# Kernel optimization log

Measured on AMD Instinct MI355X. Metric: run time of the kernel, lower is better.

## Reference

```python
import jax, jax.numpy as jnp
import numpy as np

N_NODES = 100_000
N_EDGES = 3_200_000
IN_FEAT = 512
HIDDEN = 16
N_CLASSES = 7


def setup_inputs() -> dict:
    key = jax.random.key(0)
    kx, ke, kw1, kw2 = jax.random.split(key, 4)
    x = jax.random.normal(kx, (N_NODES, IN_FEAT), dtype=jnp.float32)
    edge_index = jax.random.randint(ke, (2, N_EDGES), 0, N_NODES, dtype=jnp.int64)
    W1 = jax.random.normal(kw1, (IN_FEAT, HIDDEN), dtype=jnp.float32) * (1.0 / np.sqrt(IN_FEAT))
    b1 = jnp.zeros((HIDDEN,), dtype=jnp.float32)
    W2 = jax.random.normal(kw2, (HIDDEN, N_CLASSES), dtype=jnp.float32) * (1.0 / np.sqrt(HIDDEN))
    b2 = jnp.zeros((N_CLASSES,), dtype=jnp.float32)
    return {"x": x, "edge_index": edge_index, "W1": W1, "b1": b1, "W2": W2, "b2": b2}


def _gcn_conv(x, edge_index, W, b):
    """GCNConv: h = D^{-1/2} (A + I) D^{-1/2} (x W) + b  (symmetric normalization, self-loops)."""
    n = x.shape[0]
    h = x @ W  # transform first (small out dim), then aggregate
    loop = jnp.arange(n, dtype=edge_index.dtype)
    src = jnp.concatenate([edge_index[0], loop])  # message sources (incl. self-loops)
    dst = jnp.concatenate([edge_index[1], loop])  # message destinations
    deg = jax.ops.segment_sum(jnp.ones_like(dst, dtype=h.dtype), dst, num_segments=n)
    dinv = jnp.where(deg > 0, jax.lax.rsqrt(deg), 0.0).astype(h.dtype)
    norm = dinv[src] * dinv[dst]                 # [E+N]
    msg = h[src] * norm[:, None]                 # gather + scale
    out = jax.ops.segment_sum(msg, dst, num_segments=n)  # scatter-add
    return out + b


def reference(x, edge_index, W1, b1, W2, b2):
    h = jax.nn.relu(_gcn_conv(x, edge_index, W1, b1))
    # dropout is identity in eval mode
    logits = _gcn_conv(h, edge_index, W2, b2)
    return jax.nn.log_softmax(logits, axis=1)
```

## Files before the change

### kernel.cpp

```cpp
#include <hip/hip_runtime.h>
#include <math.h>

#define TPB 256
#define SCANT 1024

namespace {

constexpr int IN_FEAT = 512;
constexpr int HID = 16;

__device__ inline float4 shfl_xor4(float4 v, int m) {
  v.x = __shfl_xor(v.x, m);
  v.y = __shfl_xor(v.y, m);
  v.z = __shfl_xor(v.z, m);
  v.w = __shfl_xor(v.w, m);
  return v;
}

__global__ void k_detect(const int* __restrict__ ei32, int* __restrict__ flag) {
  __shared__ int red[TPB];
  int t = threadIdx.x;
  int v = 0;
  for (int i = t; i < 2048; i += TPB) v |= ei32[2 * i + 1];
  red[t] = v;
  __syncthreads();
  for (int s = TPB / 2; s > 0; s >>= 1) {
    if (t < s) red[t] |= red[t + s];
    __syncthreads();
  }
  if (t == 0) *flag = (red[0] == 0) ? 1 : 0;
}

__global__ void k_zero_i(int* __restrict__ p, int n) {
  int i = blockIdx.x * TPB + threadIdx.x;
  if (i < n) p[i] = 0;
}

__global__ __launch_bounds__(TPB) void k_binA(const int* __restrict__ ei32,
                                              const long long* __restrict__ ei64,
                                              const int* __restrict__ flag,
                                              int* __restrict__ bucketCnt, int E, int NB) {
  __shared__ int hist[1024];
  int t = threadIdx.x;
  for (int i = t; i < 1024; i += TPB) hist[i] = 0;
  __syncthreads();
  long long e0 = (long long)blockIdx.x * 8192;
  int use64 = *flag;
  for (int j = 0; j < 32; j++) {
    long long e = e0 + j * TPB + t;
    if (e < E) {
      int d = use64 ? (int)ei64[E + e] : ei32[E + e];
      atomicAdd(&hist[d >> 8], 1);
    }
  }
  __syncthreads();
  for (int b = t; b < NB; b += TPB) {
    int c = hist[b];
    if (c) atomicAdd(&bucketCnt[b], c);
  }
}

__global__ __launch_bounds__(SCANT) void k_binB(const int* __restrict__ bucketCnt,
                                                int* __restrict__ bucketBase,
                                                int* __restrict__ cursor,
                                                int* __restrict__ offsets, int n, int NB) {
  __shared__ int sb[SCANT];
  int t = threadIdx.x;
  int v = (t < NB) ? bucketCnt[t] : 0;
  sb[t] = v;
  __syncthreads();
  for (int off = 1; off < SCANT; off <<= 1) {
    int u = (t >= off) ? sb[t - off] : 0;
    __syncthreads();
    sb[t] += u;
    __syncthreads();
  }
  if (t < NB) {
    int base = sb[t] - v;
    bucketBase[t] = base;
    cursor[t] = base;
  }
  if (t == NB - 1) {
    bucketBase[NB] = sb[t];
    offsets[n] = sb[t];
  }
}

__global__ __launch_bounds__(TPB) void k_binC(const int* __restrict__ ei32,
                                              const long long* __restrict__ ei64,
                                              const int* __restrict__ flag,
                                              int* __restrict__ cursor,
                                              unsigned int* __restrict__ binned, int E, int NB) {
  __shared__ int cnt[1024];
  __shared__ int gbase[1024];
  int t = threadIdx.x;
  for (int i = t; i < 1024; i += TPB) cnt[i] = 0;
  __syncthreads();
  long long e0 = (long long)blockIdx.x * 8192;
  int use64 = *flag;
  for (int j = 0; j < 32; j++) {
    long long e = e0 + j * TPB + t;
    if (e < E) {
      int d = use64 ? (int)ei64[E + e] : ei32[E + e];
      atomicAdd(&cnt[d >> 8], 1);
    }
  }
  __syncthreads();
  for (int b = t; b < NB; b += TPB) {
    int c = cnt[b];
    gbase[b] = c ? atomicAdd(&cursor[b], c) : 0;
  }
  __syncthreads();
  for (int i = t; i < 1024; i += TPB) cnt[i] = 0;
  __syncthreads();
  for (int j = 0; j < 32; j++) {
    long long e = e0 + j * TPB + t;
    if (e < E) {
      int s, d;
      if (use64) {
        s = (int)ei64[e];
        d = (int)ei64[E + e];
      } else {
        s = ei32[e];
        d = ei32[(long long)E + e];
      }
      int b = d >> 8;
      int r = atomicAdd(&cnt[b], 1);
      binned[gbase[b] + r] = ((unsigned)(d & 255) << 24) | (unsigned)s;
    }
  }
}

__global__ __launch_bounds__(TPB) void k_binD(const int* __restrict__ bucketBase,
                                              const unsigned int* __restrict__ binned,
                                              int* __restrict__ offsets, float* __restrict__ dinv,
                                              int* __restrict__ csr, int n) {
  __shared__ int ncnt[256];
  __shared__ int nsc[256];
  __shared__ int ncur[256];
  int t = threadIdx.x;
  int b = blockIdx.x;
  int base = bucketBase[b];
  int cnt = bucketBase[b + 1] - base;
  ncnt[t] = 0;
  __syncthreads();
  for (int i = t; i < cnt; i += TPB) {
    unsigned p = binned[base + i];
    atomicAdd(&ncnt[p >> 24], 1);
  }
  __syncthreads();
  int c = ncnt[t];
  nsc[t] = c;
  __syncthreads();
  for (int off = 1; off < 256; off <<= 1) {
    int u = (t >= off) ? nsc[t - off] : 0;
    __syncthreads();
    nsc[t] += u;
    __syncthreads();
  }
  int excl = nsc[t] - c;
  int node = (b << 8) + t;
  if (node < n) {
    offsets[node] = base + excl;
    dinv[node] = rsqrtf((float)(c + 1));
  }
  ncur[t] = base + excl;
  __syncthreads();
  for (int i = t; i < cnt; i += TPB) {
    unsigned p = binned[base + i];
    int loc = (int)(p >> 24);
    int pos = atomicAdd(&ncur[loc], 1);
    csr[pos] = (int)(p & 0xFFFFFF);
  }
}

__global__ __launch_bounds__(TPB) void k_gemm1b(const float* __restrict__ x,
                                                const float* __restrict__ W1,
                                                const float* __restrict__ dinv,
                                                float* __restrict__ hs1, int n) {
  __shared__ float xs[192 * 64];
  __shared__ float wt[16 * 68];
  int t = threadIdx.x;
  int rq = t >> 2;
  int cq = t & 3;
  int R0 = blockIdx.x * 192;
  float acc[3][4];
#pragma unroll
  for (int i = 0; i < 3; i++)
#pragma unroll
    for (int c = 0; c < 4; c++) acc[i][c] = 0.f;

  const float4* x4 = (const float4*)x;
  for (int tile = 0; tile < 8; tile++) {
    int k04 = tile << 4;
#pragma unroll
    for (int p = 0; p < 12; p++) {
      int i = p * TPB + t;
      int rr = i >> 4, kk = i & 15;
      int row = R0 + rr;
      if (row > n - 1) row = n - 1;
      float4 v = x4[(long long)row * 128 + k04 + kk];
      *(float4*)&xs[((rr << 4) + (kk ^ (rr & 15))) << 2] = v;
    }
#pragma unroll
    for (int p = 0; p < 4; p++) {
      int i = p * TPB + t;
      int c = i & 15, kf = i >> 4;
      wt[c * 68 + kf] = W1[(((tile << 6) + kf) << 4) + c];
    }
    __syncthreads();
#pragma unroll 4
    for (int kk = 0; kk < 16; kk++) {
      float4 wv[4];
#pragma unroll
      for (int c = 0; c < 4; c++)
        wv[c] = *(const float4*)&wt[(cq * 4 + c) * 68 + (kk << 2)];
#pragma unroll
      for (int i = 0; i < 3; i++) {
        int rr = rq + (i << 6);
        float4 xv = *(const float4*)&xs[((rr << 4) + (kk ^ (rr & 15))) << 2];
#pragma unroll
        for (int c = 0; c < 4; c++) {
          acc[i][c] = fmaf(xv.x, wv[c].x, acc[i][c]);
          acc[i][c] = fmaf(xv.y, wv[c].y, acc[i][c]);
          acc[i][c] = fmaf(xv.z, wv[c].z, acc[i][c]);
          acc[i][c] = fmaf(xv.w, wv[c].w, acc[i][c]);
        }
      }
    }
    __syncthreads();
  }
#pragma unroll
  for (int i = 0; i < 3; i++) {
    int row = R0 + rq + (i << 6);
    if (row < n) {
      float di = dinv[row];
      float4 o = make_float4(acc[i][0] * di, acc[i][1] * di, acc[i][2] * di,
                             acc[i][3] * di);
      *(float4*)&hs1[(long long)row * HID + (cq << 2)] = o;
    }
  }
}

__global__ void k_agg1(const int* __restrict__ offsets, const int* __restrict__ csr,
                       const float* __restrict__ hs1, float* __restrict__ t1, int n) {
  int wid = (int)(((unsigned)blockIdx.x * TPB + threadIdx.x) >> 6);
  if (wid >= n) return;
  int lane = threadIdx.x & 63;
  int q = lane & 3;
  int eg = lane >> 2;
  int s0 = offsets[wid], s1 = offsets[wid + 1];
  float4 acc = make_float4(0.f, 0.f, 0.f, 0.f);
  for (int e = s0 + eg; e < s1; e += 16) {
    int s = csr[e];
    float4 v = *(const float4*)(hs1 + (long long)s * HID + (q << 2));
    acc.x += v.x; acc.y += v.y; acc.z += v.z; acc.w += v.w;
  }
  for (int m = 4; m < 64; m <<= 1) {
    float4 o = shfl_xor4(acc, m);
    acc.x += o.x; acc.y += o.y; acc.z += o.z; acc.w += o.w;
  }
  if (lane < 4) {
    float4 sv = *(const float4*)(hs1 + (long long)wid * HID + (lane << 2));
    acc.x += sv.x; acc.y += sv.y; acc.z += sv.z; acc.w += sv.w;
    *(float4*)(t1 + (long long)wid * HID + (lane << 2)) = acc;
  }
}

__global__ void k_layer2(const float* __restrict__ t1, const float* __restrict__ dinv,
                         const float* __restrict__ b1, const float* __restrict__ W2,
                         float* __restrict__ hs2, float* __restrict__ t2, int n) {
  int i = blockIdx.x * TPB + threadIdx.x;
  if (i >= n) return;
  float di = dinv[i];
  float h[16];
  const float4* tp = (const float4*)(t1 + (long long)i * 16);
#pragma unroll
  for (int q = 0; q < 4; q++) {
    float4 v = tp[q];
    float4 b = ((const float4*)b1)[q];
    h[4 * q + 0] = fmaxf(fmaf(di, v.x, b.x), 0.f);
    h[4 * q + 1] = fmaxf(fmaf(di, v.y, b.y), 0.f);
    h[4 * q + 2] = fmaxf(fmaf(di, v.z, b.z), 0.f);
    h[4 * q + 3] = fmaxf(fmaf(di, v.w, b.w), 0.f);
  }
  float o[8];
#pragma unroll
  for (int j = 0; j < 7; j++) {
    float s = 0.f;
#pragma unroll
    for (int cc = 0; cc < 16; cc++) s = fmaf(h[cc], W2[cc * 7 + j], s);
    o[j] = s * di;
  }
  o[7] = 0.f;
  float4 lo = make_float4(o[0], o[1], o[2], o[3]);
  float4 hi = make_float4(o[4], o[5], o[6], o[7]);
  float4* hp = (float4*)(hs2 + (long long)i * 8);
  hp[0] = lo; hp[1] = hi;
  if (t2) {
    float4* qp = (float4*)(t2 + (long long)i * 8);
    qp[0] = lo; qp[1] = hi;
  }
}

__global__ void k_agg2(const int* __restrict__ offsets, const int* __restrict__ csr,
                       const float* __restrict__ hs2, const float* __restrict__ dinv,
                       const float* __restrict__ b2, float* __restrict__ out, int n) {
  int wid = (int)(((unsigned)blockIdx.x * TPB + threadIdx.x) >> 6);
  if (wid >= n) return;
  int lane = threadIdx.x & 63;
  int q = lane & 1;
  int eg = lane >> 1;
  int s0 = offsets[wid], s1 = offsets[wid + 1];
  float4 acc = make_float4(0.f, 0.f, 0.f, 0.f);
  for (int e = s0 + eg; e < s1; e += 32) {
    int s = csr[e];
    float4 v = *(const float4*)(hs2 + (long long)s * 8 + (q << 2));
    acc.x += v.x; acc.y += v.y; acc.z += v.z; acc.w += v.w;
  }
  for (int m = 2; m < 64; m <<= 1) {
    float4 o = shfl_xor4(acc, m);
    acc.x += o.x; acc.y += o.y; acc.z += o.z; acc.w += o.w;
  }
  float4 sv = *(const float4*)(hs2 + (long long)wid * 8 + (q << 2));
  acc.x += sv.x; acc.y += sv.y; acc.z += sv.z; acc.w += sv.w;
  float di = dinv[wid];
  int f0 = q << 2;
  float vx = fmaf(di, acc.x, b2[f0 + 0]);
  float vy = fmaf(di, acc.y, b2[f0 + 1]);
  float vz = fmaf(di, acc.z, b2[f0 + 2]);
  float vw = (q == 0) ? fmaf(di, acc.w, b2[3]) : 0.f;
  float vw_eff = (q == 0) ? vw : -1e30f;
  float mloc = fmaxf(fmaxf(vx, vy), fmaxf(vz, vw_eff));
  float mm = fmaxf(mloc, __shfl_xor(mloc, 1));
  float sl = expf(vx - mm) + expf(vy - mm) + expf(vz - mm) +
             ((q == 0) ? expf(vw - mm) : 0.f);
  float ss = sl + __shfl_xor(sl, 1);
  float lse = mm + logf(ss);
  if (lane < 2) {
    long long base = (long long)wid * 7 + (q << 2);
    out[base + 0] = vx - lse;
    out[base + 1] = vy - lse;
    out[base + 2] = vz - lse;
    if (q == 0) out[base + 3] = vw - lse;
  }
}

__global__ void k_hist(const int* __restrict__ ei32, const long long* __restrict__ ei64,
                       const int* __restrict__ flag, int* __restrict__ cnt, int E) {
  int e = blockIdx.x * TPB + threadIdx.x;
  if (e >= E) return;
  int d = (*flag) ? (int)ei64[(long long)E + e] : ei32[(long long)E + e];
  atomicAdd(&cnt[d], 1);
}

__global__ __launch_bounds__(SCANT) void k_scan(int* __restrict__ cnt_cursor,
                                                int* __restrict__ offsets,
                                                float* __restrict__ dinv, int n) {
  __shared__ int sb[SCANT];
  int t = threadIdx.x;
  int chunk = (n + SCANT - 1) / SCANT;
  int lo = t * chunk;
  int hi = lo + chunk;
  if (lo > n) lo = n;
  if (hi > n) hi = n;
  int s = 0;
  for (int i = lo; i < hi; i++) s += cnt_cursor[i];
  sb[t] = s;
  __syncthreads();
  for (int off = 1; off < SCANT; off <<= 1) {
    int v = (t >= off) ? sb[t - off] : 0;
    __syncthreads();
    sb[t] += v;
    __syncthreads();
  }
  int run = sb[t] - s;
  for (int i = lo; i < hi; i++) {
    int c = cnt_cursor[i];
    offsets[i] = run;
    cnt_cursor[i] = run;
    dinv[i] = rsqrtf((float)(c + 1));
    run += c;
  }
  if (hi == n && lo < n) offsets[n] = run;
}

__global__ void k_build(const int* __restrict__ ei32, const long long* __restrict__ ei64,
                        const int* __restrict__ flag, int* __restrict__ cursor,
                        int* __restrict__ csr, int E) {
  int e = blockIdx.x * TPB + threadIdx.x;
  if (e >= E) return;
  int s, d;
  if (*flag) {
    s = (int)ei64[e];
    d = (int)ei64[(long long)E + e];
  } else {
    s = ei32[e];
    d = ei32[(long long)E + e];
  }
  int pos = atomicAdd(&cursor[d], 1);
  csr[pos] = s;
}

__global__ __launch_bounds__(TPB) void k_gemm1(const float* __restrict__ x,
                                               const float* __restrict__ W1,
                                               const float* __restrict__ dinv,
                                               float* __restrict__ hs1,
                                               float* __restrict__ t1, int n) {
  __shared__ float Wt[HID * IN_FEAT];
  __shared__ float xsl[16 * IN_FEAT];
  int t = threadIdx.x;
  for (int i = t; i < IN_FEAT * HID; i += TPB) {
    int k = i >> 4, c = i & 15;
    int pk = (k >> 2) ^ (c & 7);
    Wt[c * IN_FEAT + (pk << 2) + (k & 3)] = W1[i];
  }
  int c = t >> 4, r = t & 15;
  int xsw = r & 7, wsw = c & 7;
  int ntiles = (n + 15) >> 4;
  for (int tile = blockIdx.x; tile < ntiles; tile += gridDim.x) {
    int r0 = tile << 4;
    for (int i = t; i < 16 * (IN_FEAT / 4); i += TPB) {
      int rr = i >> 7, kk = i & 127;
      int row = r0 + rr;
      if (row > n - 1) row = n - 1;
      float4 v = ((const float4*)x)[(long long)row * (IN_FEAT / 4) + kk];
      *(float4*)&xsl[rr * IN_FEAT + ((kk ^ (rr & 7)) << 2)] = v;
    }
    __syncthreads();
    float acc = 0.f;
#pragma unroll 8
    for (int kk = 0; kk < IN_FEAT / 4; kk++) {
      float4 xv = *(const float4*)&xsl[r * IN_FEAT + ((kk ^ xsw) << 2)];
      float4 wv = *(const float4*)&Wt[c * IN_FEAT + ((kk ^ wsw) << 2)];
      acc = fmaf(xv.x, wv.x, acc);
      acc = fmaf(xv.y, wv.y, acc);
      acc = fmaf(xv.z, wv.z, acc);
      acc = fmaf(xv.w, wv.w, acc);
    }
    int row = r0 + r;
    if (row < n) {
      float val = acc * dinv[row];
      hs1[(long long)row * HID + c] = val;
      if (t1) t1[(long long)row * HID + c] = val;
    }
    __syncthreads();
  }
}

__global__ void k_deg_init(float* __restrict__ deg, int n) {
  int i = blockIdx.x * TPB + threadIdx.x;
  if (i < n) deg[i] = 1.0f;
}

__global__ void k_deg_accum(const int* __restrict__ ei32, const long long* __restrict__ ei64,
                            const int* __restrict__ flag, float* __restrict__ deg, int E) {
  int e = blockIdx.x * TPB + threadIdx.x;
  if (e >= E) return;
  int d = (*flag) ? (int)ei64[(long long)E + e] : ei32[(long long)E + e];
  atomicAdd(&deg[d], 1.0f);
}

__global__ void k_rsqrt(float* __restrict__ deg, int n) {
  int i = blockIdx.x * TPB + threadIdx.x;
  if (i < n) deg[i] = rsqrtf(deg[i]);
}

__global__ void k_scatter1(const int* __restrict__ ei32, const long long* __restrict__ ei64,
                           const int* __restrict__ flag, const float* __restrict__ hs1,
                           float* __restrict__ t1, int E) {
  long long gid = (long long)blockIdx.x * TPB + threadIdx.x;
  long long e = gid >> 4;
  if (e >= E) return;
  int f = (int)(gid & 15);
  int s, d;
  if (*flag) {
    s = (int)ei64[e];
    d = (int)ei64[E + e];
  } else {
    s = ei32[e];
    d = ei32[(long long)E + e];
  }
  atomicAdd(&t1[(long long)d * HID + f], hs1[(long long)s * HID + f]);
}

__global__ void k_scatter2(const int* __restrict__ ei32, const long long* __restrict__ ei64,
                           const int* __restrict__ flag, const float* __restrict__ hs2,
                           float* __restrict__ t2, int E) {
  long long gid = (long long)blockIdx.x * TPB + threadIdx.x;
  long long e = gid >> 3;
  if (e >= E) return;
  int f = (int)(gid & 7);
  if (f == 7) return;
  int s, d;
  if (*flag) {
    s = (int)ei64[e];
    d = (int)ei64[E + e];
  } else {
    s = ei32[e];
    d = ei32[(long long)E + e];
  }
  atomicAdd(&t2[(long long)d * 8 + f], hs2[(long long)s * 8 + f]);
}

__global__ void k_final(const float* __restrict__ t2, const float* __restrict__ dinv,
                        const float* __restrict__ b2, float* __restrict__ out, int n) {
  int i = blockIdx.x * TPB + threadIdx.x;
  if (i >= n) return;
  float di = dinv[i];
  float v[7];
  float m = -1e30f;
#pragma unroll
  for (int j = 0; j < 7; j++) {
    v[j] = fmaf(di, t2[(long long)i * 8 + j], b2[j]);
    m = fmaxf(m, v[j]);
  }
  float s = 0.f;
#pragma unroll
  for (int j = 0; j < 7; j++) s += expf(v[j] - m);
  float lse = m + logf(s);
#pragma unroll
  for (int j = 0; j < 7; j++) out[(long long)i * 7 + j] = v[j] - lse;
}

}

extern "C" void kernel_launch(void* const* d_in, const int* in_sizes, int n_in,
                              void* d_out, int out_size, void* d_ws, size_t ws_size,
                              hipStream_t stream) {
  const float* x = (const float*)d_in[0];
  const int* ei32 = (const int*)d_in[1];
  const long long* ei64 = (const long long*)d_in[1];
  const float* W1 = (const float*)d_in[2];
  const float* b1 = (const float*)d_in[3];
  const float* W2 = (const float*)d_in[4];
  const float* b2 = (const float*)d_in[5];
  float* out = (float*)d_out;

  int n = in_sizes[0] / IN_FEAT;
  int E = in_sizes[1] / 2;

  int nb_n = (n + TPB - 1) / TPB;
  int nb_e = (E + TPB - 1) / TPB;
  int nb_w = (n + 3) / 4;
  int nb_g = (n + 191) / 192;
  int NB = (n + 255) >> 8;
  int NCH = (int)(((long long)E + 8191) / 8192);

  float* ws = (float*)d_ws;
  int* flag = (int*)d_ws;
  auto align16 = [](long long v) { return (v + 15) & ~15LL; };

  long long w = 64;
  float* dinv = ws + w; w = align16(w + n);
  int* offsets = (int*)(ws + w); w = align16(w + n + 1);
  int* bucketCnt = (int*)(ws + w); w = align16(w + NB);
  int* bucketBase = (int*)(ws + w); w = align16(w + NB + 1);
  int* cursor = (int*)(ws + w); w = align16(w + NB);
  unsigned int* binned = (unsigned int*)(ws + w); w = align16(w + E);
  int* csr = (int*)(ws + w); w = align16(w + E);
  float* hs1 = ws + w; w = align16(w + (long long)n * HID);
  float* t1 = ws + w; w = align16(w + (long long)n * HID);
  float* hs2 = ws + w; w = align16(w + (long long)n * 8);
  bool bin_ok = (NB >= 1) && (NB <= 1024) && (n <= (1 << 24)) &&
                (ws_size >= (size_t)w * 4);

  long long w2l = 64;
  float* dinv_c = ws + w2l; w2l = align16(w2l + n);
  int* offsets_c = (int*)(ws + w2l); w2l = align16(w2l + n + 1);
  int* cursor_c = (int*)(ws + w2l); w2l = align16(w2l + n);
  int* csr_c = (int*)(ws + w2l); w2l = align16(w2l + E);
  float* hs1_c = ws + w2l; w2l = align16(w2l + (long long)n * HID);
  float* t1_c = ws + w2l; w2l = align16(w2l + (long long)n * HID);
  float* hs2_c = ws + w2l; w2l = align16(w2l + (long long)n * 8);
  bool csr_ok = (ws_size >= (size_t)w2l * 4);

  if (bin_ok) {
    int nb_nb = (NB + TPB - 1) / TPB;
    hipLaunchKernelGGL(k_detect, dim3(1), dim3(TPB), 0, stream, ei32, flag);
    hipLaunchKernelGGL(k_zero_i, dim3(nb_nb), dim3(TPB), 0, stream, bucketCnt, NB);
    hipLaunchKernelGGL(k_binA, dim3(NCH), dim3(TPB), 0, stream, ei32, ei64, flag, bucketCnt, E, NB);
    hipLaunchKernelGGL(k_binB, dim3(1), dim3(SCANT), 0, stream, bucketCnt, bucketBase, cursor,
                       offsets, n, NB);
    hipLaunchKernelGGL(k_binC, dim3(NCH), dim3(TPB), 0, stream, ei32, ei64, flag, cursor, binned,
                       E, NB);
    hipLaunchKernelGGL(k_binD, dim3(NB), dim3(TPB), 0, stream, bucketBase, binned, offsets, dinv,
                       csr, n);
    hipLaunchKernelGGL(k_gemm1b, dim3(nb_g), dim3(TPB), 0, stream, x, W1, dinv, hs1, n);
    hipLaunchKernelGGL(k_agg1, dim3(nb_w), dim3(TPB), 0, stream, offsets, csr, hs1, t1, n);
    hipLaunchKernelGGL(k_layer2, dim3(nb_n), dim3(TPB), 0, stream, t1, dinv, b1, W2, hs2,
                       (float*)nullptr, n);
    hipLaunchKernelGGL(k_agg2, dim3(nb_w), dim3(TPB), 0, stream, offsets, csr, hs2, dinv, b2,
                       out, n);
  } else if (csr_ok) {
    hipLaunchKernelGGL(k_detect, dim3(1), dim3(TPB), 0, stream, ei32, flag);
    hipLaunchKernelGGL(k_zero_i, dim3(nb_n), dim3(TPB), 0, stream, cursor_c, n);
    hipLaunchKernelGGL(k_hist, dim3(nb_e), dim3(TPB), 0, stream, ei32, ei64, flag, cursor_c, E);
    hipLaunchKernelGGL(k_scan, dim3(1), dim3(SCANT), 0, stream, cursor_c, offsets_c, dinv_c, n);
    hipLaunchKernelGGL(k_build, dim3(nb_e), dim3(TPB), 0, stream, ei32, ei64, flag, cursor_c,
                       csr_c, E);
    hipLaunchKernelGGL(k_gemm1b, dim3(nb_g), dim3(TPB), 0, stream, x, W1, dinv_c, hs1_c, n);
    hipLaunchKernelGGL(k_agg1, dim3(nb_w), dim3(TPB), 0, stream, offsets_c, csr_c, hs1_c, t1_c, n);
    hipLaunchKernelGGL(k_layer2, dim3(nb_n), dim3(TPB), 0, stream, t1_c, dinv_c, b1, W2, hs2_c,
                       (float*)nullptr, n);
    hipLaunchKernelGGL(k_agg2, dim3(nb_w), dim3(TPB), 0, stream, offsets_c, csr_c, hs2_c, dinv_c,
                       b2, out, n);
  } else {
    float* dinv_f = ws + 64;
    float* hs1_f = dinv_f + n;
    float* t1_f = hs1_f + (long long)n * HID;
    float* hs2_f = t1_f + (long long)n * HID;
    float* t2_f = hs2_f + (long long)n * 8;
    long long w1s = (long long)E * 16, w2s = (long long)E * 8;
    int nb_s1 = (int)((w1s + TPB - 1) / TPB);
    int nb_s2 = (int)((w2s + TPB - 1) / TPB);
    hipLaunchKernelGGL(k_detect, dim3(1), dim3(TPB), 0, stream, ei32, flag);
    hipLaunchKernelGGL(k_deg_init, dim3(nb_n), dim3(TPB), 0, stream, dinv_f, n);
    hipLaunchKernelGGL(k_deg_accum, dim3(nb_e), dim3(TPB), 0, stream, ei32, ei64, flag, dinv_f, E);
    hipLaunchKernelGGL(k_rsqrt, dim3(nb_n), dim3(TPB), 0, stream, dinv_f, n);
    hipLaunchKernelGGL(k_gemm1, dim3(1024), dim3(TPB), 0, stream, x, W1, dinv_f, hs1_f, t1_f, n);
    hipLaunchKernelGGL(k_scatter1, dim3(nb_s1), dim3(TPB), 0, stream, ei32, ei64, flag, hs1_f,
                       t1_f, E);
    hipLaunchKernelGGL(k_layer2, dim3(nb_n), dim3(TPB), 0, stream, t1_f, dinv_f, b1, W2, hs2_f,
                       t2_f, n);
    hipLaunchKernelGGL(k_scatter2, dim3(nb_s2), dim3(TPB), 0, stream, ei32, ei64, flag, hs2_f,
                       t2_f, E);
    hipLaunchKernelGGL(k_final, dim3(nb_n), dim3(TPB), 0, stream, t2_f, dinv_f, b2, out, n);
  }
}
```

Measured before the change: 523.5 us.

## Aggregate directly from bucketed edges with LDS atomics, dropping CSR build

Replaces the per-node CSR construction (k_binD) with a lighter degree-only kernel and switches the bucket size from 256 to 128 nodes. Both aggregation passes now read the bucket-binned edge list directly and accumulate into shared-memory tiles with LDS float atomics. The layer-2 transform is fused into the first aggregation, and log-softmax into the second. This removes the CSR scatter pass, the t1 buffer and the separate layer2 launch, at the cost of shared-memory atomic contention and nondeterministic float summation order.

```diff
diff --git a/kernel.cpp b/kernel.cpp
--- a/kernel.cpp
+++ b/kernel.cpp
@@ -8,14 +8,8 @@
 
 constexpr int IN_FEAT = 512;
 constexpr int HID = 16;
-
-__device__ inline float4 shfl_xor4(float4 v, int m) {
-  v.x = __shfl_xor(v.x, m);
-  v.y = __shfl_xor(v.y, m);
-  v.z = __shfl_xor(v.z, m);
-  v.w = __shfl_xor(v.w, m);
-  return v;
-}
+constexpr int BSH = 7;
+constexpr int BSZ = 128;
 
 __global__ void k_detect(const int* __restrict__ ei32, int* __restrict__ flag) {
   __shared__ int red[TPB];
@@ -50,7 +44,7 @@
     long long e = e0 + j * TPB + t;
     if (e < E) {
       int d = use64 ? (int)ei64[E + e] : ei32[E + e];
-      atomicAdd(&hist[d >> 8], 1);
+      atomicAdd(&hist[d >> BSH], 1);
     }
   }
   __syncthreads();
@@ -62,8 +56,7 @@
 
 __global__ __launch_bounds__(SCANT) void k_binB(const int* __restrict__ bucketCnt,
                                                 int* __restrict__ bucketBase,
-                                                int* __restrict__ cursor,
-                                                int* __restrict__ offsets, int n, int NB) {
+                                                int* __restrict__ cursor, int NB) {
   __shared__ int sb[SCANT];
   int t = threadIdx.x;
   int v = (t < NB) ? bucketCnt[t] : 0;
@@ -80,10 +73,7 @@
     bucketBase[t] = base;
     cursor[t] = base;
   }
-  if (t == NB - 1) {
-    bucketBase[NB] = sb[t];
-    offsets[n] = sb[t];
-  }
+  if (t == NB - 1) bucketBase[NB] = sb[t];
 }
 
 __global__ __launch_bounds__(TPB) void k_binC(const int* __restrict__ ei32,
@@ -102,7 +92,7 @@
     long long e = e0 + j * TPB + t;
     if (e < E) {
       int d = use64 ? (int)ei64[E + e] : ei32[E + e];
-      atomicAdd(&cnt[d >> 8], 1);
+      atomicAdd(&cnt[d >> BSH], 1);
     }
   }
   __syncthreads();
@@ -124,54 +114,26 @@
         s = ei32[e];
         d = ei32[(long long)E + e];
       }
-      int b = d >> 8;
+      int b = d >> BSH;
       int r = atomicAdd(&cnt[b], 1);
-      binned[gbase[b] + r] = ((unsigned)(d & 255) << 24) | (unsigned)s;
-    }
-  }
-}
-
-__global__ __launch_bounds__(TPB) void k_binD(const int* __restrict__ bucketBase,
+      binned[gbase[b] + r] = ((unsigned)(d & (BSZ - 1)) << 25) | (unsigned)s;
+    }
+  }
+}
+
+__global__ __launch_bounds__(TPB) void k_dinv(const int* __restrict__ bucketBase,
                                               const unsigned int* __restrict__ binned,
-                                              int* __restrict__ offsets, float* __restrict__ dinv,
-                                              int* __restrict__ csr, int n) {
-  __shared__ int ncnt[256];
-  __shared__ int nsc[256];
-  __shared__ int ncur[256];
-  int t = threadIdx.x;
-  int b = blockIdx.x;
+                                              float* __restrict__ dinv, int n) {
+  __shared__ int ncnt[BSZ];
+  int t = threadIdx.x, b = blockIdx.x;
   int base = bucketBase[b];
   int cnt = bucketBase[b + 1] - base;
-  ncnt[t] = 0;
-  __syncthreads();
-  for (int i = t; i < cnt; i += TPB) {
-    unsigned p = binned[base + i];
-    atomicAdd(&ncnt[p >> 24], 1);
-  }
-  __syncthreads();
-  int c = ncnt[t];
-  nsc[t] = c;
-  __syncthreads();
-  for (int off = 1; off < 256; off <<= 1) {
-    int u = (t >= off) ? nsc[t - off] : 0;
-    __syncthreads();
-    nsc[t] += u;
-    __syncthreads();
-  }
-  int excl = nsc[t] - c;
-  int node = (b << 8) + t;
-  if (node < n) {
-    offsets[node] = base + excl;
-    dinv[node] = rsqrtf((float)(c + 1));
-  }
-  ncur[t] = base + excl;
-  __syncthreads();
-  for (int i = t; i < cnt; i += TPB) {
-    unsigned p = binned[base + i];
-    int loc = (int)(p >> 24);
-    int pos = atomicAdd(&ncur[loc], 1);
-    csr[pos] = (int)(p & 0xFFFFFF);
-  }
+  if (t < BSZ) ncnt[t] = 0;
+  __syncthreads();
+  for (int i = t; i < cnt; i += TPB) atomicAdd(&ncnt[binned[base + i] >> 25], 1);
+  __syncthreads();
+  int node = (b << BSH) + t;
+  if (t < BSZ && node < n) dinv[node] = rsqrtf((float)(ncnt[t] + 1));
 }
 
 __global__ __launch_bounds__(TPB) void k_gemm1b(const float* __restrict__ x,
@@ -242,164 +204,106 @@
   }
 }
 
-__global__ void k_agg1(const int* __restrict__ offsets, const int* __restrict__ csr,
-                       const float* __restrict__ hs1, float* __restrict__ t1, int n) {
-  int wid = (int)(((unsigned)blockIdx.x * TPB + threadIdx.x) >> 6);
-  if (wid >= n) return;
-  int lane = threadIdx.x & 63;
-  int q = lane & 3;
-  int eg = lane >> 2;
-  int s0 = offsets[wid], s1 = offsets[wid + 1];
-  float4 acc = make_float4(0.f, 0.f, 0.f, 0.f);
-  for (int e = s0 + eg; e < s1; e += 16) {
-    int s = csr[e];
-    float4 v = *(const float4*)(hs1 + (long long)s * HID + (q << 2));
-    acc.x += v.x; acc.y += v.y; acc.z += v.z; acc.w += v.w;
-  }
-  for (int m = 4; m < 64; m <<= 1) {
-    float4 o = shfl_xor4(acc, m);
-    acc.x += o.x; acc.y += o.y; acc.z += o.z; acc.w += o.w;
-  }
-  if (lane < 4) {
-    float4 sv = *(const float4*)(hs1 + (long long)wid * HID + (lane << 2));
-    acc.x += sv.x; acc.y += sv.y; acc.z += sv.z; acc.w += sv.w;
-    *(float4*)(t1 + (long long)wid * HID + (lane << 2)) = acc;
-  }
-}
-
-__global__ void k_layer2(const float* __restrict__ t1, const float* __restrict__ dinv,
-                         const float* __restrict__ b1, const float* __restrict__ W2,
-                         float* __restrict__ hs2, float* __restrict__ t2, int n) {
-  int i = blockIdx.x * TPB + threadIdx.x;
-  if (i >= n) return;
-  float di = dinv[i];
-  float h[16];
-  const float4* tp = (const float4*)(t1 + (long long)i * 16);
-#pragma unroll
-  for (int q = 0; q < 4; q++) {
-    float4 v = tp[q];
-    float4 b = ((const float4*)b1)[q];
-    h[4 * q + 0] = fmaxf(fmaf(di, v.x, b.x), 0.f);
-    h[4 * q + 1] = fmaxf(fmaf(di, v.y, b.y), 0.f);
-    h[4 * q + 2] = fmaxf(fmaf(di, v.z, b.z), 0.f);
-    h[4 * q + 3] = fmaxf(fmaf(di, v.w, b.w), 0.f);
-  }
-  float o[8];
-#pragma unroll
-  for (int j = 0; j < 7; j++) {
-    float s = 0.f;
-#pragma unroll
-    for (int cc = 0; cc < 16; cc++) s = fmaf(h[cc], W2[cc * 7 + j], s);
-    o[j] = s * di;
-  }
-  o[7] = 0.f;
-  float4 lo = make_float4(o[0], o[1], o[2], o[3]);
-  float4 hi = make_float4(o[4], o[5], o[6], o[7]);
-  float4* hp = (float4*)(hs2 + (long long)i * 8);
-  hp[0] = lo; hp[1] = hi;
-  if (t2) {
-    float4* qp = (float4*)(t2 + (long long)i * 8);
-    qp[0] = lo; qp[1] = hi;
-  }
-}
-
-__global__ void k_agg2(const int* __restrict__ offsets, const int* __restrict__ csr,
-                       const float* __restrict__ hs2, const float* __restrict__ dinv,
-                       const float* __restrict__ b2, float* __restrict__ out, int n) {
-  int wid = (int)(((unsigned)blockIdx.x * TPB + threadIdx.x) >> 6);
-  if (wid >= n) return;
-  int lane = threadIdx.x & 63;
-  int q = lane & 1;
-  int eg = lane >> 1;
-  int s0 = offsets[wid], s1 = offsets[wid + 1];
-  float4 acc = make_float4(0.f, 0.f, 0.f, 0.f);
-  for (int e = s0 + eg; e < s1; e += 32) {
-    int s = csr[e];
-    float4 v = *(const float4*)(hs2 + (long long)s * 8 + (q << 2));
-    acc.x += v.x; acc.y += v.y; acc.z += v.z; acc.w += v.w;
-  }
-  for (int m = 2; m < 64; m <<= 1) {
-    float4 o = shfl_xor4(acc, m);
-    acc.x += o.x; acc.y += o.y; acc.z += o.z; acc.w += o.w;
-  }
-  float4 sv = *(const float4*)(hs2 + (long long)wid * 8 + (q << 2));
-  acc.x += sv.x; acc.y += sv.y; acc.z += sv.z; acc.w += sv.w;
-  float di = dinv[wid];
-  int f0 = q << 2;
-  float vx = fmaf(di, acc.x, b2[f0 + 0]);
-  float vy = fmaf(di, acc.y, b2[f0 + 1]);
-  float vz = fmaf(di, acc.z, b2[f0 + 2]);
-  float vw = (q == 0) ? fmaf(di, acc.w, b2[3]) : 0.f;
-  float vw_eff = (q == 0) ? vw : -1e30f;
-  float mloc = fmaxf(fmaxf(vx, vy), fmaxf(vz, vw_eff));
-  float mm = fmaxf(mloc, __shfl_xor(mloc, 1));
-  float sl = expf(vx - mm) + expf(vy - mm) + expf(vz - mm) +
-             ((q == 0) ? expf(vw - mm) : 0.f);
-  float ss = sl + __shfl_xor(sl, 1);
-  float lse = mm + logf(ss);
-  if (lane < 2) {
-    long long base = (long long)wid * 7 + (q << 2);
-    out[base + 0] = vx - lse;
-    out[base + 1] = vy - lse;
-    out[base + 2] = vz - lse;
-    if (q == 0) out[base + 3] = vw - lse;
-  }
-}
-
-__global__ void k_hist(const int* __restrict__ ei32, const long long* __restrict__ ei64,
-                       const int* __restrict__ flag, int* __restrict__ cnt, int E) {
-  int e = blockIdx.x * TPB + threadIdx.x;
-  if (e >= E) return;
-  int d = (*flag) ? (int)ei64[(long long)E + e] : ei32[(long long)E + e];
-  atomicAdd(&cnt[d], 1);
-}
-
-__global__ __launch_bounds__(SCANT) void k_scan(int* __restrict__ cnt_cursor,
-                                                int* __restrict__ offsets,
-                                                float* __restrict__ dinv, int n) {
-  __shared__ int sb[SCANT];
-  int t = threadIdx.x;
-  int chunk = (n + SCANT - 1) / SCANT;
-  int lo = t * chunk;
-  int hi = lo + chunk;
-  if (lo > n) lo = n;
-  if (hi > n) hi = n;
-  int s = 0;
-  for (int i = lo; i < hi; i++) s += cnt_cursor[i];
-  sb[t] = s;
-  __syncthreads();
-  for (int off = 1; off < SCANT; off <<= 1) {
-    int v = (t >= off) ? sb[t - off] : 0;
-    __syncthreads();
-    sb[t] += v;
-    __syncthreads();
-  }
-  int run = sb[t] - s;
-  for (int i = lo; i < hi; i++) {
-    int c = cnt_cursor[i];
-    offsets[i] = run;
-    cnt_cursor[i] = run;
-    dinv[i] = rsqrtf((float)(c + 1));
-    run += c;
-  }
-  if (hi == n && lo < n) offsets[n] = run;
-}
-
-__global__ void k_build(const int* __restrict__ ei32, const long long* __restrict__ ei64,
-                        const int* __restrict__ flag, int* __restrict__ cursor,
-                        int* __restrict__ csr, int E) {
-  int e = blockIdx.x * TPB + threadIdx.x;
-  if (e >= E) return;
-  int s, d;
-  if (*flag) {
-    s = (int)ei64[e];
-    d = (int)ei64[(long long)E + e];
-  } else {
-    s = ei32[e];
-    d = ei32[(long long)E + e];
-  }
-  int pos = atomicAdd(&cursor[d], 1);
-  csr[pos] = s;
+__global__ __launch_bounds__(TPB) void k_fagg1(const int* __restrict__ bucketBase,
+                                               const unsigned int* __restrict__ binned,
+                                               const float* __restrict__ hs1,
+                                               const float* __restrict__ dinv,
+                                               const float* __restrict__ b1,
+                                               const float* __restrict__ W2,
+                                               float* __restrict__ hs2, int n) {
+  __shared__ float acc[BSZ * 17];
+  int t = threadIdx.x, b = blockIdx.x;
+  int base = bucketBase[b];
+  int cnt = bucketBase[b + 1] - base;
+  for (int i = t; i < BSZ * 17; i += TPB) acc[i] = 0.f;
+  __syncthreads();
+  int work = cnt << 2;
+  for (int i = t; i < work; i += TPB) {
+    unsigned p = binned[base + (i >> 2)];
+    int q = i & 3;
+    int loc = (int)(p >> 25);
+    int s = (int)(p & 0x1FFFFFF);
+    float4 v = *(const float4*)(hs1 + ((long long)s << 4) + (q << 2));
+    float* a = &acc[loc * 17 + (q << 2)];
+    atomicAdd(&a[0], v.x);
+    atomicAdd(&a[1], v.y);
+    atomicAdd(&a[2], v.z);
+    atomicAdd(&a[3], v.w);
+  }
+  __syncthreads();
+  int node = (b << BSH) + t;
+  if (t < BSZ && node < n) {
+    float di = dinv[node];
+    const float4* sp = (const float4*)(hs1 + ((long long)node << 4));
+    float h[16];
+#pragma unroll
+    for (int qq = 0; qq < 4; qq++) {
+      float4 sv = sp[qq];
+      float4 bb = ((const float4*)b1)[qq];
+      const float* a = &acc[t * 17 + (qq << 2)];
+      h[4 * qq + 0] = fmaxf(fmaf(di, a[0] + sv.x, bb.x), 0.f);
+      h[4 * qq + 1] = fmaxf(fmaf(di, a[1] + sv.y, bb.y), 0.f);
+      h[4 * qq + 2] = fmaxf(fmaf(di, a[2] + sv.z, bb.z), 0.f);
+      h[4 * qq + 3] = fmaxf(fmaf(di, a[3] + sv.w, bb.w), 0.f);
+    }
+    float o[8];
+#pragma unroll
+    for (int j = 0; j < 7; j++) {
+      float s2 = 0.f;
+#pragma unroll
+      for (int cc = 0; cc < 16; cc++) s2 = fmaf(h[cc], W2[cc * 7 + j], s2);
+      o[j] = s2 * di;
+    }
+    o[7] = 0.f;
+    float4* hp = (float4*)(hs2 + ((long long)node << 3));
+    hp[0] = make_float4(o[0], o[1], o[2], o[3]);
+    hp[1] = make_float4(o[4], o[5], o[6], o[7]);
+  }
+}
+
+__global__ __launch_bounds__(TPB) void k_fagg2(const int* __restrict__ bucketBase,
+                                               const unsigned int* __restrict__ binned,
+                                               const float* __restrict__ hs2,
+                                               const float* __restrict__ dinv,
+                                               const float* __restrict__ b2,
+                                               float* __restrict__ out, int n) {
+  __shared__ float acc[BSZ * 9];
+  int t = threadIdx.x, b = blockIdx.x;
+  int base = bucketBase[b];
+  int cnt = bucketBase[b + 1] - base;
+  for (int i = t; i < BSZ * 9; i += TPB) acc[i] = 0.f;
+  __syncthreads();
+  int work = cnt << 1;
+  for (int i = t; i < work; i += TPB) {
+    unsigned p = binned[base + (i >> 1)];
+    int q = i & 1;
+    int loc = (int)(p >> 25);
+    int s = (int)(p & 0x1FFFFFF);
+    float4 v = *(const float4*)(hs2 + ((long long)s << 3) + (q << 2));
+    float* a = &acc[loc * 9 + (q << 2)];
+    atomicAdd(&a[0], v.x);
+    atomicAdd(&a[1], v.y);
+    atomicAdd(&a[2], v.z);
+    atomicAdd(&a[3], v.w);
+  }
+  __syncthreads();
+  int node = (b << BSH) + t;
+  if (t < BSZ && node < n) {
+    float di = dinv[node];
+    const float* sp = hs2 + ((long long)node << 3);
+    float v[7], m = -1e30f;
+#pragma unroll
+    for (int j = 0; j < 7; j++) {
+      v[j] = fmaf(di, acc[t * 9 + j] + sp[j], b2[j]);
+      m = fmaxf(m, v[j]);
+    }
+    float ssum = 0.f;
+#pragma unroll
+    for (int j = 0; j < 7; j++) ssum += expf(v[j] - m);
+    float lse = m + logf(ssum);
+#pragma unroll
+    for (int j = 0; j < 7; j++) out[(long long)node * 7 + j] = v[j] - lse;
+  }
 }
 
 __global__ __launch_bounds__(TPB) void k_gemm1(const float* __restrict__ x,
@@ -482,6 +386,42 @@
     d = ei32[(long long)E + e];
   }
   atomicAdd(&t1[(long long)d * HID + f], hs1[(long long)s * HID + f]);
+}
+
+__global__ void k_layer2(const float* __restrict__ t1, const float* __restrict__ dinv,
+                         const float* __restrict__ b1, const float* __restrict__ W2,
+                         float* __restrict__ hs2, float* __restrict__ t2, int n) {
+  int i = blockIdx.x * TPB + threadIdx.x;
+  if (i >= n) return;
+  float di = dinv[i];
+  float h[16];
+  const float4* tp = (const float4*)(t1 + (long long)i * 16);
+#pragma unroll
+  for (int q = 0; q < 4; q++) {
+    float4 v = tp[q];
+    float4 b = ((const float4*)b1)[q];
+    h[4 * q + 0] = fmaxf(fmaf(di, v.x, b.x), 0.f);
+    h[4 * q + 1] = fmaxf(fmaf(di, v.y, b.y), 0.f);
+    h[4 * q + 2] = fmaxf(fmaf(di, v.z, b.z), 0.f);
+    h[4 * q + 3] = fmaxf(fmaf(di, v.w, b.w), 0.f);
+  }
+  float o[8];
+#pragma unroll
+  for (int j = 0; j < 7; j++) {
+    float s = 0.f;
+#pragma unroll
+    for (int cc = 0; cc < 16; cc++) s = fmaf(h[cc], W2[cc * 7 + j], s);
+    o[j] = s * di;
+  }
+  o[7] = 0.f;
+  float4 lo = make_float4(o[0], o[1], o[2], o[3]);
+  float4 hi = make_float4(o[4], o[5], o[6], o[7]);
+  float4* hp = (float4*)(hs2 + (long long)i * 8);
+  hp[0] = lo; hp[1] = hi;
+  if (t2) {
+    float4* qp = (float4*)(t2 + (long long)i * 8);
+    qp[0] = lo; qp[1] = hi;
+  }
 }
 
 __global__ void k_scatter2(const int* __restrict__ ei32, const long long* __restrict__ ei64,
@@ -542,9 +482,8 @@
 
   int nb_n = (n + TPB - 1) / TPB;
   int nb_e = (E + TPB - 1) / TPB;
-  int nb_w = (n + 3) / 4;
   int nb_g = (n + 191) / 192;
-  int NB = (n + 255) >> 8;
+  int NB = (n + BSZ - 1) >> BSH;
   int NCH = (int)(((long long)E + 8191) / 8192);
 
   float* ws = (float*)d_ws;
@@ -553,57 +492,30 @@
 
   long long w = 64;
   float* dinv = ws + w; w = align16(w + n);
-  int* offsets = (int*)(ws + w); w = align16(w + n + 1);
   int* bucketCnt = (int*)(ws + w); w = align16(w + NB);
   int* bucketBase = (int*)(ws + w); w = align16(w + NB + 1);
   int* cursor = (int*)(ws + w); w = align16(w + NB);
   unsigned int* binned = (unsigned int*)(ws + w); w = align16(w + E);
-  int* csr = (int*)(ws + w); w = align16(w + E);
   float* hs1 = ws + w; w = align16(w + (long long)n * HID);
-  float* t1 = ws + w; w = align16(w + (long long)n * HID);
   float* hs2 = ws + w; w = align16(w + (long long)n * 8);
-  bool bin_ok = (NB >= 1) && (NB <= 1024) && (n <= (1 << 24)) &&
+  bool bin_ok = (NB >= 1) && (NB <= 1024) && (n <= (1 << 25)) &&
                 (ws_size >= (size_t)w * 4);
-
-  long long w2l = 64;
-  float* dinv_c = ws + w2l; w2l = align16(w2l + n);
-  int* offsets_c = (int*)(ws + w2l); w2l = align16(w2l + n + 1);
-  int* cursor_c = (int*)(ws + w2l); w2l = align16(w2l + n);
-  int* csr_c = (int*)(ws + w2l); w2l = align16(w2l + E);
-  float* hs1_c = ws + w2l; w2l = align16(w2l + (long long)n * HID);
-  float* t1_c = ws + w2l; w2l = align16(w2l + (long long)n * HID);
-  float* hs2_c = ws + w2l; w2l = align16(w2l + (long long)n * 8);
-  bool csr_ok = (ws_size >= (size_t)w2l * 4);
 
   if (bin_ok) {
     int nb_nb = (NB + TPB - 1) / TPB;
     hipLaunchKernelGGL(k_detect, dim3(1), dim3(TPB), 0, stream, ei32, flag);
     hipLaunchKernelGGL(k_zero_i, dim3(nb_nb), dim3(TPB), 0, stream, bucketCnt, NB);
-    hipLaunchKernelGGL(k_binA, dim3(NCH), dim3(TPB), 0, stream, ei32, ei64, flag, bucketCnt, E, NB);
+    hipLaunchKernelGGL(k_binA, dim3(NCH), dim3(TPB), 0, stream, ei32, ei64, flag, bucketCnt, E,
+                       NB);
     hipLaunchKernelGGL(k_binB, dim3(1), dim3(SCANT), 0, stream, bucketCnt, bucketBase, cursor,
-                       offsets, n, NB);
+                       NB);
     hipLaunchKernelGGL(k_binC, dim3(NCH), dim3(TPB), 0, stream, ei32, ei64, flag, cursor, binned,
                        E, NB);
-    hipLaunchKernelGGL(k_binD, dim3(NB), dim3(TPB), 0, stream, bucketBase, binned, offsets, dinv,
-                       csr, n);
+    hipLaunchKernelGGL(k_dinv, dim3(NB), dim3(TPB), 0, stream, bucketBase, binned, dinv, n);
     hipLaunchKernelGGL(k_gemm1b, dim3(nb_g), dim3(TPB), 0, stream, x, W1, dinv, hs1, n);
-    hipLaunchKernelGGL(k_agg1, dim3(nb_w), dim3(TPB), 0, stream, offsets, csr, hs1, t1, n);
-    hipLaunchKernelGGL(k_layer2, dim3(nb_n), dim3(TPB), 0, stream, t1, dinv, b1, W2, hs2,
-                       (float*)nullptr, n);
-    hipLaunchKernelGGL(k_agg2, dim3(nb_w), dim3(TPB), 0, stream, offsets, csr, hs2, dinv, b2,
-                       out, n);
-  } else if (csr_ok) {
-    hipLaunchKernelGGL(k_detect, dim3(1), dim3(TPB), 0, stream, ei32, flag);
-    hipLaunchKernelGGL(k_zero_i, dim3(nb_n), dim3(TPB), 0, stream, cursor_c, n);
-    hipLaunchKernelGGL(k_hist, dim3(nb_e), dim3(TPB), 0, stream, ei32, ei64, flag, cursor_c, E);
-    hipLaunchKernelGGL(k_scan, dim3(1), dim3(SCANT), 0, stream, cursor_c, offsets_c, dinv_c, n);
-    hipLaunchKernelGGL(k_build, dim3(nb_e), dim3(TPB), 0, stream, ei32, ei64, flag, cursor_c,
-                       csr_c, E);
-    hipLaunchKernelGGL(k_gemm1b, dim3(nb_g), dim3(TPB), 0, stream, x, W1, dinv_c, hs1_c, n);
-    hipLaunchKernelGGL(k_agg1, dim3(nb_w), dim3(TPB), 0, stream, offsets_c, csr_c, hs1_c, t1_c, n);
-    hipLaunchKernelGGL(k_layer2, dim3(nb_n), dim3(TPB), 0, stream, t1_c, dinv_c, b1, W2, hs2_c,
-                       (float*)nullptr, n);
-    hipLaunchKernelGGL(k_agg2, dim3(nb_w), dim3(TPB), 0, stream, offsets_c, csr_c, hs2_c, dinv_c,
+    hipLaunchKernelGGL(k_fagg1, dim3(NB), dim3(TPB), 0, stream, bucketBase, binned, hs1, dinv,
+                       b1, W2, hs2, n);
+    hipLaunchKernelGGL(k_fagg2, dim3(NB), dim3(TPB), 0, stream, bucketBase, binned, hs2, dinv,
                        b2, out, n);
   } else {
     float* dinv_f = ws + 64;
@@ -616,7 +528,8 @@
     int nb_s2 = (int)((w2s + TPB - 1) / TPB);
     hipLaunchKernelGGL(k_detect, dim3(1), dim3(TPB), 0, stream, ei32, flag);
     hipLaunchKernelGGL(k_deg_init, dim3(nb_n), dim3(TPB), 0, stream, dinv_f, n);
-    hipLaunchKernelGGL(k_deg_accum, dim3(nb_e), dim3(TPB), 0, stream, ei32, ei64, flag, dinv_f, E);
+    hipLaunchKernelGGL(k_deg_accum, dim3(nb_e), dim3(TPB), 0, stream, ei32, ei64, flag, dinv_f,
+                       E);
     hipLaunchKernelGGL(k_rsqrt, dim3(nb_n), dim3(TPB), 0, stream, dinv_f, n);
     hipLaunchKernelGGL(k_gemm1, dim3(1024), dim3(TPB), 0, stream, x, W1, dinv_f, hs1_f, t1_f, n);
     hipLaunchKernelGGL(k_scatter1, dim3(nb_s1), dim3(TPB), 0, stream, ei32, ei64, flag, hs1_f,
```

After: 929.9 us. +77.6%, slower.
